# Kernel optimization log

Hardware: AMD Instinct MI355X
Metric: run time of the kernel (lower is better)

Reference implementation:

```python
import jax, jax.numpy as jnp
import numpy as np


def _gcn_conv(x, W, b, row, col, norm, num_nodes):
    # PyG GCNConv: transform then normalized sum-aggregate over edges (incl. self loops)
    xw = x @ W                                   # [N, F_out]
    msg = xw[row] * norm[:, None]                # gather + scale, [E+N, F_out]
    agg = jax.ops.segment_sum(msg, col, num_segments=num_nodes)
    return agg + b


def setup_inputs() -> dict:
    key = jax.random.key(0)
    ks = jax.random.split(key, 10)
    N, E, F_in, H = 100000, 1600000, 128, 128
    Hh = H // 2
    x = jax.random.normal(ks[0], (N, F_in), dtype=jnp.float32)
    edge_index = jax.random.randint(ks[1], (2, E), 0, N, dtype=jnp.int64)
    def glorot(k, shape):
        lim = float(np.sqrt(6.0 / (shape[0] + shape[1])))
        return jax.random.uniform(k, shape, dtype=jnp.float32, minval=-lim, maxval=lim)
    return {
        "x": x,
        "edge_index": edge_index,
        "W1": glorot(ks[2], (F_in, Hh)), "b1": jnp.zeros((Hh,), jnp.float32),
        "Wf1": glorot(ks[3], (F_in, Hh)), "bf1": jnp.zeros((Hh,), jnp.float32),
        "W2": glorot(ks[4], (H, 1)), "b2": jnp.zeros((1,), jnp.float32),
        "Wf2": glorot(ks[5], (H, 1)), "bf2": jnp.zeros((1,), jnp.float32),
    }


def reference(x, edge_index, W1, b1, Wf1, bf1, W2, b2, Wf2, bf2):
    N = x.shape[0]
    loop = jnp.arange(N, dtype=edge_index.dtype)
    row = jnp.concatenate([edge_index[0], loop])   # sources
    col = jnp.concatenate([edge_index[1], loop])   # targets
    # symmetric normalization D^{-1/2} (A+I) D^{-1/2}, degree on target nodes
    deg = jax.ops.segment_sum(jnp.ones_like(col, dtype=x.dtype), col, num_segments=N)
    dinv = jnp.where(deg > 0, jax.lax.rsqrt(deg), 0.0)
    norm = dinv[row] * dinv[col]                   # [E+N]
    h = jnp.concatenate([
        _gcn_conv(x, W1, b1, row, col, norm, N),
        x @ Wf1 + bf1,
    ], axis=1)
    h = jax.nn.relu(h)
    # dropout is identity in eval mode
    out = _gcn_conv(h, W2, b2, row, col, norm, N) + (h @ Wf2 + bf2)
    return out.reshape(-1)
```

## Files before the change

kernel.cpp:

```cpp
#include <hip/hip_runtime.h>
#include <hip/hip_fp16.h>

constexpr int FIN   = 128;
constexpr int HH    = 64;
constexpr int NPB   = 256;
constexpr int MAXNB = 512;
constexpr int BCH   = 4096;
constexpr int BCAP  = 4608;
constexpr int CAPB  = 4500;

typedef _Float16 half4v __attribute__((ext_vector_type(4)));

__global__ __launch_bounds__(256) void k_gemm(
    const float* __restrict__ x, const float* __restrict__ W1,
    const float* __restrict__ Wf1, _Float16* __restrict__ xwh, int N)
{
    __shared__ float xs[16][68];
    __shared__ float ws[16][128];

    const int tid = threadIdx.x;
    const int tx  = tid & 31;
    const int ty  = tid >> 5;
    const int nbase = blockIdx.x * 64;

    float acc[8][4];
#pragma unroll
    for (int i = 0; i < 8; ++i)
#pragma unroll
        for (int j = 0; j < 4; ++j) acc[i][j] = 0.0f;

    const int xr_row = tid >> 2;
    const int xr_kk0 = (tid & 3) * 4;
    int nload = nbase + xr_row;
    const int nclamped = (nload < N) ? nload : (N - 1);

    const int wk = tid >> 4;
    const int wc = (tid * 8) & 127;

    for (int k0 = 0; k0 < FIN; k0 += 16) {
        float4 xv = *(const float4*)(x + (size_t)nclamped * FIN + k0 + xr_kk0);
        xs[xr_kk0 + 0][xr_row] = xv.x;
        xs[xr_kk0 + 1][xr_row] = xv.y;
        xs[xr_kk0 + 2][xr_row] = xv.z;
        xs[xr_kk0 + 3][xr_row] = xv.w;
        {
            const float* src = (wc < HH) ? (W1  + (size_t)(k0 + wk) * HH + wc)
                                         : (Wf1 + (size_t)(k0 + wk) * HH + (wc - HH));
            float4 w0 = *(const float4*)(src);
            float4 w1 = *(const float4*)(src + 4);
            *(float4*)&ws[wk][wc]     = w0;
            *(float4*)&ws[wk][wc + 4] = w1;
        }
        __syncthreads();

#pragma unroll
        for (int kk = 0; kk < 16; ++kk) {
            float4 xa = *(const float4*)&xs[kk][ty * 8];
            float4 xb = *(const float4*)&xs[kk][ty * 8 + 4];
            float4 wv = *(const float4*)&ws[kk][tx * 4];
            float xr[8] = {xa.x, xa.y, xa.z, xa.w, xb.x, xb.y, xb.z, xb.w};
#pragma unroll
            for (int i = 0; i < 8; ++i) {
                acc[i][0] = fmaf(xr[i], wv.x, acc[i][0]);
                acc[i][1] = fmaf(xr[i], wv.y, acc[i][1]);
                acc[i][2] = fmaf(xr[i], wv.z, acc[i][2]);
                acc[i][3] = fmaf(xr[i], wv.w, acc[i][3]);
            }
        }
        __syncthreads();
    }

#pragma unroll
    for (int i = 0; i < 8; ++i) {
        int n = nbase + ty * 8 + i;
        if (n < N) {
            half4v h;
            h[0] = (_Float16)acc[i][0]; h[1] = (_Float16)acc[i][1];
            h[2] = (_Float16)acc[i][2]; h[3] = (_Float16)acc[i][3];
            *(half4v*)(xwh + (size_t)n * FIN + tx * 4) = h;
        }
    }
}

__global__ __launch_bounds__(256) void k_bin(
    const int* __restrict__ ei, int* __restrict__ bcur,
    int2* __restrict__ binned, int E, int NB)
{
    __shared__ int hist[MAXNB], scur[MAXNB], gbase[MAXNB], sbase[MAXNB];
    __shared__ int ssum[256];
    __shared__ int2 st[BCH];
    const int tid = threadIdx.x;
    const int e0  = blockIdx.x * BCH;
    const int nE  = min(BCH, E - e0);

    for (int b = tid; b < NB; b += 256) hist[b] = 0;
    __syncthreads();

    for (int k = tid; k < nE; k += 256)
        atomicAdd(&hist[ei[E + e0 + k] >> 8], 1);
    __syncthreads();

    int h0 = (2 * tid     < NB) ? hist[2 * tid]     : 0;
    int h1 = (2 * tid + 1 < NB) ? hist[2 * tid + 1] : 0;
    ssum[tid] = h0 + h1;
    __syncthreads();
    for (int o = 1; o < 256; o <<= 1) {
        int y = (tid >= o) ? ssum[tid - o] : 0;
        __syncthreads();
        ssum[tid] += y;
        __syncthreads();
    }
    int eb = ssum[tid] - h0 - h1;
    if (2 * tid     < NB) { sbase[2 * tid]     = eb;      scur[2 * tid]     = eb; }
    if (2 * tid + 1 < NB) { sbase[2 * tid + 1] = eb + h0; scur[2 * tid + 1] = eb + h0; }
    __syncthreads();

    for (int b = tid; b < NB; b += 256)
        if (hist[b] > 0) gbase[b] = atomicAdd(bcur + b, hist[b]);

    for (int k = tid; k < nE; k += 256) {
        int r = ei[e0 + k];
        int c = ei[E + e0 + k];
        int s = atomicAdd(&scur[c >> 8], 1);
        st[s] = make_int2(r, c);
    }
    __syncthreads();

    for (int s = tid; s < nE; s += 256) {
        int2 rc = st[s];
        int b = rc.y >> 8;
        long dest = (long)b * BCAP + gbase[b] + (s - sbase[b]);
        binned[dest] = rc;
    }
}

__global__ __launch_bounds__(256) void k_bscan(
    const int* __restrict__ bcur, int* __restrict__ bbase, int NB)
{
    __shared__ int s[256];
    const int t = threadIdx.x;
    int a = (2 * t     < NB) ? bcur[2 * t]     : 0;
    int b = (2 * t + 1 < NB) ? bcur[2 * t + 1] : 0;
    s[t] = a + b;
    __syncthreads();
    for (int o = 1; o < 256; o <<= 1) {
        int y = (t >= o) ? s[t - o] : 0;
        __syncthreads();
        s[t] += y;
        __syncthreads();
    }
    int excl = s[t] - a - b;
    if (2 * t     < NB) bbase[2 * t]     = excl;
    if (2 * t + 1 < NB) bbase[2 * t + 1] = excl + a;
}

__global__ __launch_bounds__(256) void k_place(
    const int2* __restrict__ binned, const int* __restrict__ bcur,
    const int* __restrict__ bbase, int* __restrict__ cnt, int* __restrict__ off,
    float* __restrict__ dinv, int* __restrict__ sedge, int N)
{
    const int b   = blockIdx.x;
    const int tid = threadIdx.x;
    const int nlo = b << 8;
    const int nn  = min(NPB, N - nlo);
    __shared__ int lcnt[NPB], loff[NPB], lscan[NPB];
    __shared__ int stage[CAPB];
    lcnt[tid] = 0;
    __syncthreads();
    const int ke = bcur[b];
    const int2* src = binned + (long)b * BCAP;
    for (int k = tid; k < ke; k += 256)
        atomicAdd(&lcnt[src[k].y - nlo], 1);
    __syncthreads();
    int v = lcnt[tid];
    lscan[tid] = v;
    __syncthreads();
    for (int o = 1; o < 256; o <<= 1) {
        int y = (tid >= o) ? lscan[tid - o] : 0;
        __syncthreads();
        lscan[tid] += y;
        __syncthreads();
    }
    int excl = lscan[tid] - v;
    loff[tid] = excl;
    const int base = bbase[b];
    if (tid < nn) {
        cnt[nlo + tid]  = v;
        off[nlo + tid]  = base + excl;
        dinv[nlo + tid] = rsqrtf((float)v + 1.0f);
    }
    lcnt[tid] = 0;
    __syncthreads();
    if (ke <= CAPB) {
        for (int k = tid; k < ke; k += 256) {
            int2 rc = src[k];
            int li = rc.y - nlo;
            int p = atomicAdd(&lcnt[li], 1);
            stage[loff[li] + p] = rc.x;
        }
        __syncthreads();
        for (int s = tid; s < ke; s += 256) sedge[base + s] = stage[s];
    } else {
        for (int k = tid; k < ke; k += 256) {
            int2 rc = src[k];
            int li = rc.y - nlo;
            int p = atomicAdd(&lcnt[li], 1);
            sedge[base + loff[li] + p] = rc.x;
        }
    }
}

__global__ __launch_bounds__(256) void k_fused(
    const int* __restrict__ off, const int* __restrict__ cnt,
    const int* __restrict__ sedge, const float* __restrict__ dinv,
    const _Float16* __restrict__ xwh,
    const float* __restrict__ b1, const float* __restrict__ bf1,
    const float* __restrict__ W2, const float* __restrict__ Wf2,
    const float* __restrict__ b2, const float* __restrict__ bf2,
    float* __restrict__ z, float* __restrict__ out, int N)
{
    const int wv   = (blockIdx.x * blockDim.x + threadIdx.x) >> 6;
    const int lane = threadIdx.x & 63;
    const int g    = lane >> 4;
    const int l16  = lane & 15;
    int i = wv * 4 + g;
    const bool ok = (i < N);
    i = ok ? i : (N - 1);

    const int jb  = off[i];
    const int deg = cnt[i];
    const float di = dinv[i];

    float4 acc = make_float4(0.f, 0.f, 0.f, 0.f);
    int j = 0;
    for (; j + 4 <= deg; j += 4) {
        int r0 = sedge[jb + j];
        int r1 = sedge[jb + j + 1];
        int r2 = sedge[jb + j + 2];
        int r3 = sedge[jb + j + 3];
        float s0 = dinv[r0] * di;
        float s1 = dinv[r1] * di;
        float s2 = dinv[r2] * di;
        float s3 = dinv[r3] * di;
        half4v a0 = *(const half4v*)(xwh + (size_t)r0 * FIN + l16 * 4);
        half4v a1 = *(const half4v*)(xwh + (size_t)r1 * FIN + l16 * 4);
        half4v a2 = *(const half4v*)(xwh + (size_t)r2 * FIN + l16 * 4);
        half4v a3 = *(const half4v*)(xwh + (size_t)r3 * FIN + l16 * 4);
        acc.x = fmaf((float)a0[0], s0, acc.x);
        acc.y = fmaf((float)a0[1], s0, acc.y);
        acc.z = fmaf((float)a0[2], s0, acc.z);
        acc.w = fmaf((float)a0[3], s0, acc.w);
        acc.x = fmaf((float)a1[0], s1, acc.x);
        acc.y = fmaf((float)a1[1], s1, acc.y);
        acc.z = fmaf((float)a1[2], s1, acc.z);
        acc.w = fmaf((float)a1[3], s1, acc.w);
        acc.x = fmaf((float)a2[0], s2, acc.x);
        acc.y = fmaf((float)a2[1], s2, acc.y);
        acc.z = fmaf((float)a2[2], s2, acc.z);
        acc.w = fmaf((float)a2[3], s2, acc.w);
        acc.x = fmaf((float)a3[0], s3, acc.x);
        acc.y = fmaf((float)a3[1], s3, acc.y);
        acc.z = fmaf((float)a3[2], s3, acc.z);
        acc.w = fmaf((float)a3[3], s3, acc.w);
    }
    for (; j < deg; ++j) {
        int r = sedge[jb + j];
        float s = dinv[r] * di;
        half4v a = *(const half4v*)(xwh + (size_t)r * FIN + l16 * 4);
        acc.x = fmaf((float)a[0], s, acc.x);
        acc.y = fmaf((float)a[1], s, acc.y);
        acc.z = fmaf((float)a[2], s, acc.z);
        acc.w = fmaf((float)a[3], s, acc.w);
    }

    float dd = di * di;
    half4v svh = *(const half4v*)(xwh + (size_t)i * FIN + l16 * 4);
    acc.x = fmaf((float)svh[0], dd, acc.x);
    acc.y = fmaf((float)svh[1], dd, acc.y);
    acc.z = fmaf((float)svh[2], dd, acc.z);
    acc.w = fmaf((float)svh[3], dd, acc.w);

    float4 b1v  = *(const float4*)(b1  + l16 * 4);
    float4 bf1v = *(const float4*)(bf1 + l16 * 4);
    half4v x1h  = *(const half4v*)(xwh + (size_t)i * FIN + HH + l16 * 4);
    float4 h0, h1;
    h0.x = fmaxf(acc.x + b1v.x, 0.f);  h0.y = fmaxf(acc.y + b1v.y, 0.f);
    h0.z = fmaxf(acc.z + b1v.z, 0.f);  h0.w = fmaxf(acc.w + b1v.w, 0.f);
    h1.x = fmaxf((float)x1h[0] + bf1v.x, 0.f);  h1.y = fmaxf((float)x1h[1] + bf1v.y, 0.f);
    h1.z = fmaxf((float)x1h[2] + bf1v.z, 0.f);  h1.w = fmaxf((float)x1h[3] + bf1v.w, 0.f);

    float4 w2a  = *(const float4*)(W2  + l16 * 4);
    float4 w2b  = *(const float4*)(W2  + HH + l16 * 4);
    float4 wf2a = *(const float4*)(Wf2 + l16 * 4);
    float4 wf2b = *(const float4*)(Wf2 + HH + l16 * 4);

    float zp = h0.x * w2a.x + h0.y * w2a.y + h0.z * w2a.z + h0.w * w2a.w
             + h1.x * w2b.x + h1.y * w2b.y + h1.z * w2b.z + h1.w * w2b.w;
    float fp = h0.x * wf2a.x + h0.y * wf2a.y + h0.z * wf2a.z + h0.w * wf2a.w
             + h1.x * wf2b.x + h1.y * wf2b.y + h1.z * wf2b.z + h1.w * wf2b.w;
#pragma unroll
    for (int o = 8; o > 0; o >>= 1) {
        zp += __shfl_xor(zp, o, 16);
        fp += __shfl_xor(fp, o, 16);
    }
    if (l16 == 0 && ok) {
        z[i]   = zp;
        out[i] = fp + b2[0] + bf2[0];
    }
}

__global__ __launch_bounds__(256) void k_agg2(
    const int* __restrict__ off, const int* __restrict__ cnt,
    const int* __restrict__ sedge, const float* __restrict__ dinv,
    const float* __restrict__ z, float* __restrict__ out, int N)
{
    const int wid  = (blockIdx.x * blockDim.x + threadIdx.x) >> 6;
    const int lane = threadIdx.x & 63;
    const int g    = lane >> 4;
    const int l16  = lane & 15;
    int i = wid * 4 + g;
    bool ok = (i < N);
    i = ok ? i : (N - 1);

    const int jb = off[i], je = jb + cnt[i];
    float s = 0.0f;
    for (int j = jb + l16; j < je; j += 16) {
        int r = sedge[j];
        s = fmaf(z[r], dinv[r], s);
    }
#pragma unroll
    for (int o = 8; o > 0; o >>= 1) s += __shfl_xor(s, o, 64);
    if (l16 == 0 && ok) {
        float di = dinv[i];
        out[i] += di * fmaf(z[i], di, s);
    }
}

extern "C" void kernel_launch(void* const* d_in, const int* in_sizes, int n_in,
                              void* d_out, int out_size, void* d_ws, size_t ws_size,
                              hipStream_t stream)
{
    const float* x   = (const float*)d_in[0];
    const int*   ei  = (const int*)d_in[1];
    const float* W1  = (const float*)d_in[2];
    const float* b1  = (const float*)d_in[3];
    const float* Wf1 = (const float*)d_in[4];
    const float* bf1 = (const float*)d_in[5];
    const float* W2  = (const float*)d_in[6];
    const float* b2  = (const float*)d_in[7];
    const float* Wf2 = (const float*)d_in[8];
    const float* bf2 = (const float*)d_in[9];

    const int N = in_sizes[0] / FIN;
    const int E = in_sizes[1] / 2;
    const int NB = (N + NPB - 1) / NPB;
    float* out = (float*)d_out;

    float* ws   = (float*)d_ws;
    float* dinv = ws;
    float* z    = dinv + N;
    int*   cnt  = (int*)(z + N);
    int*   bcur = cnt + N;
    int*   bbase = bcur + MAXNB;
    int*   off  = bbase + MAXNB;
    int*   sedge = off + N;
    _Float16* xwh = (_Float16*)(sedge + E);
    int2*  binned = (int2*)(xwh + (size_t)N * FIN);

    hipMemsetAsync(bcur, 0, (size_t)MAXNB * sizeof(int), stream);

    k_bin<<<(E + BCH - 1) / BCH, 256, 0, stream>>>(ei, bcur, binned, E, NB);
    k_bscan<<<1, 256, 0, stream>>>(bcur, bbase, NB);
    k_place<<<NB, 256, 0, stream>>>(binned, bcur, bbase, cnt, off, dinv, sedge, N);

    k_gemm<<<(N + 63) / 64, 256, 0, stream>>>(x, W1, Wf1, xwh, N);

    {
        long waves = ((long)N + 3) / 4;
        int blocks = (int)((waves * 64 + 255) / 256);
        k_fused<<<blocks, 256, 0, stream>>>(off, cnt, sedge, dinv, xwh,
                                            b1, bf1, W2, Wf2, b2, bf2, z, out, N);
    }

    {
        long waves = ((long)N + 3) / 4;
        int blocks = (int)((waves * 64 + 255) / 256);
        k_agg2<<<blocks, 256, 0, stream>>>(off, cnt, sedge, dinv, z, out, N);
    }
}
```

Measured before the change: 232.9 us.

## Use MFMA f16 instructions for the input projection GEMM with swizzled LDS weights

Replaces the scalar FP32 tiled GEMM for x@[W1|Wf1] with MFMA 16x16x32 f16 matrix instructions. Each block stages the full 128x128 weight matrix as f16 in LDS with an XOR swizzle to avoid bank conflicts. Each wave converts its 16 input rows to f16 fragments held in registers. This cuts FP32 FMA work in the GEMM. In exchange, inputs are rounded to f16 before multiplication, which lowers precision, and the output stores become scalar 2-byte writes instead of vectorized ones.

```diff
diff --git a/kernel.cpp b/kernel.cpp
--- a/kernel.cpp
+++ b/kernel.cpp
@@ -10,74 +10,63 @@
 constexpr int CAPB  = 4500;
 
 typedef _Float16 half4v __attribute__((ext_vector_type(4)));
+typedef _Float16 half8v __attribute__((ext_vector_type(8)));
+typedef float    f32x4 __attribute__((ext_vector_type(4)));
 
 __global__ __launch_bounds__(256) void k_gemm(
     const float* __restrict__ x, const float* __restrict__ W1,
     const float* __restrict__ Wf1, _Float16* __restrict__ xwh, int N)
 {
-    __shared__ float xs[16][68];
-    __shared__ float ws[16][128];
+    __shared__ _Float16 wt[128 * 128];
 
     const int tid = threadIdx.x;
-    const int tx  = tid & 31;
-    const int ty  = tid >> 5;
-    const int nbase = blockIdx.x * 64;
-
-    float acc[8][4];
-#pragma unroll
-    for (int i = 0; i < 8; ++i)
-#pragma unroll
-        for (int j = 0; j < 4; ++j) acc[i][j] = 0.0f;
-
-    const int xr_row = tid >> 2;
-    const int xr_kk0 = (tid & 3) * 4;
-    int nload = nbase + xr_row;
-    const int nclamped = (nload < N) ? nload : (N - 1);
-
-    const int wk = tid >> 4;
-    const int wc = (tid * 8) & 127;
-
-    for (int k0 = 0; k0 < FIN; k0 += 16) {
-        float4 xv = *(const float4*)(x + (size_t)nclamped * FIN + k0 + xr_kk0);
-        xs[xr_kk0 + 0][xr_row] = xv.x;
-        xs[xr_kk0 + 1][xr_row] = xv.y;
-        xs[xr_kk0 + 2][xr_row] = xv.z;
-        xs[xr_kk0 + 3][xr_row] = xv.w;
-        {
-            const float* src = (wc < HH) ? (W1  + (size_t)(k0 + wk) * HH + wc)
-                                         : (Wf1 + (size_t)(k0 + wk) * HH + (wc - HH));
-            float4 w0 = *(const float4*)(src);
-            float4 w1 = *(const float4*)(src + 4);
-            *(float4*)&ws[wk][wc]     = w0;
-            *(float4*)&ws[wk][wc + 4] = w1;
+    for (int idx = tid; idx < 128 * 128; idx += 256) {
+        int n = idx & 127, k = idx >> 7;
+        float v = (n < HH) ? W1[k * HH + n] : Wf1[k * HH + (n - HH)];
+        int g  = k >> 3, j = k & 7;
+        int pg = g ^ (n & 7);
+        wt[n * 128 + pg * 8 + j] = (_Float16)v;
+    }
+    __syncthreads();
+
+    const int w  = tid >> 6;
+    const int l  = tid & 63;
+    const int rb = blockIdx.x * 64 + w * 16;
+
+    int arow = rb + (l & 15);
+    arow = (arow < N) ? arow : (N - 1);
+    half8v af[4];
+#pragma unroll
+    for (int ks = 0; ks < 4; ++ks) {
+        const float* src = x + (size_t)arow * FIN + ks * 32 + (l >> 4) * 8;
+        float4 x0 = *(const float4*)(src);
+        float4 x1 = *(const float4*)(src + 4);
+        half8v a;
+        a[0] = (_Float16)x0.x; a[1] = (_Float16)x0.y;
+        a[2] = (_Float16)x0.z; a[3] = (_Float16)x0.w;
+        a[4] = (_Float16)x1.x; a[5] = (_Float16)x1.y;
+        a[6] = (_Float16)x1.z; a[7] = (_Float16)x1.w;
+        af[ks] = a;
+    }
+
+    const int orow0 = rb + (l >> 4) * 4;
+#pragma unroll
+    for (int c = 0; c < 8; ++c) {
+        f32x4 acc = {0.f, 0.f, 0.f, 0.f};
+        const int n = (l & 15) + c * 16;
+#pragma unroll
+        for (int ks = 0; ks < 4; ++ks) {
+            int g  = ks * 4 + (l >> 4);
+            int pg = g ^ (n & 7);
+            half8v bf = *(const half8v*)(wt + n * 128 + pg * 8);
+            acc = __builtin_amdgcn_mfma_f32_16x16x32_f16(af[ks], bf, acc, 0, 0, 0);
         }
-        __syncthreads();
-
-#pragma unroll
-        for (int kk = 0; kk < 16; ++kk) {
-            float4 xa = *(const float4*)&xs[kk][ty * 8];
-            float4 xb = *(const float4*)&xs[kk][ty * 8 + 4];
-            float4 wv = *(const float4*)&ws[kk][tx * 4];
-            float xr[8] = {xa.x, xa.y, xa.z, xa.w, xb.x, xb.y, xb.z, xb.w};
-#pragma unroll
-            for (int i = 0; i < 8; ++i) {
-                acc[i][0] = fmaf(xr[i], wv.x, acc[i][0]);
-                acc[i][1] = fmaf(xr[i], wv.y, acc[i][1]);
-                acc[i][2] = fmaf(xr[i], wv.z, acc[i][2]);
-                acc[i][3] = fmaf(xr[i], wv.w, acc[i][3]);
-            }
-        }
-        __syncthreads();
-    }
-
-#pragma unroll
-    for (int i = 0; i < 8; ++i) {
-        int n = nbase + ty * 8 + i;
-        if (n < N) {
-            half4v h;
-            h[0] = (_Float16)acc[i][0]; h[1] = (_Float16)acc[i][1];
-            h[2] = (_Float16)acc[i][2]; h[3] = (_Float16)acc[i][3];
-            *(half4v*)(xwh + (size_t)n * FIN + tx * 4) = h;
+        const int ocol = c * 16 + (l & 15);
+#pragma unroll
+        for (int r = 0; r < 4; ++r) {
+            int orow = orow0 + r;
+            if (orow < N)
+                xwh[(size_t)orow * FIN + ocol] = (_Float16)acc[r];
         }
     }
 }
```

Measured after the change: 212.9 us. 8.6% less time.
